# Kernel tuning notes

Hardware: AMD Instinct MI355X
Metric: run time of the kernel (lower is better)

## Reference

```python
import jax, jax.numpy as jnp
import numpy as np

INPUT_SIZE = 64
HIDDEN = 512
NUM_CLASSES = 10


def setup_inputs() -> dict:
    key = jax.random.key(0)
    ks = jax.random.split(key, 9)
    B, T = 1024, 256
    bound_lstm = 1.0 / np.sqrt(HIDDEN)
    bound_lin = 1.0 / np.sqrt(HIDDEN)
    x = jax.random.normal(ks[0], (B, T * INPUT_SIZE), dtype=jnp.float32)
    h0 = jax.random.normal(ks[1], (B, HIDDEN), dtype=jnp.float32)
    c0 = jax.random.normal(ks[2], (B, HIDDEN), dtype=jnp.float32)
    W_ih = jax.random.uniform(ks[3], (4 * HIDDEN, INPUT_SIZE), jnp.float32, -bound_lstm, bound_lstm)
    W_hh = jax.random.uniform(ks[4], (4 * HIDDEN, HIDDEN), jnp.float32, -bound_lstm, bound_lstm)
    b_ih = jax.random.uniform(ks[5], (4 * HIDDEN,), jnp.float32, -bound_lstm, bound_lstm)
    b_hh = jax.random.uniform(ks[6], (4 * HIDDEN,), jnp.float32, -bound_lstm, bound_lstm)
    W_lin = jax.random.uniform(ks[7], (NUM_CLASSES, HIDDEN), jnp.float32, -bound_lin, bound_lin)
    b_lin = jax.random.uniform(ks[8], (NUM_CLASSES,), jnp.float32, -bound_lin, bound_lin)
    return {"x": x, "h0": h0, "c0": c0, "W_ih": W_ih, "W_hh": W_hh,
            "b_ih": b_ih, "b_hh": b_hh, "W_lin": W_lin, "b_lin": b_lin}


def _lstm_forward(x, h0, c0, W_ih, W_hh, b_ih, b_hh, W_lin, b_lin):
    B = x.shape[0]
    T = x.shape[1] // INPUT_SIZE
    # [B, T*in] -> [T, B, in]; torch.split along dim 1 gives contiguous chunks
    xs = x.reshape(B, T, INPUT_SIZE).transpose(1, 0, 2)
    # precompute input projections for all steps: [T, B, 4H]
    gates_x = jnp.einsum('tbi,gi->tbg', xs, W_ih) + b_ih + b_hh

    def step(carry, gx):
        h, c = carry
        gates = gx + h @ W_hh.T  # [B, 4H], torch gate order i,f,g,o
        i, f, g, o = jnp.split(gates, 4, axis=-1)
        i = jax.nn.sigmoid(i)
        f = jax.nn.sigmoid(f)
        g = jnp.tanh(g)
        o = jax.nn.sigmoid(o)
        c_new = f * c + i * g
        h_new = o * jnp.tanh(c_new)
        return (h_new, c_new), None

    (hT, cT), _ = jax.lax.scan(step, (h0, c0), gates_x)
    preds = hT @ W_lin.T + b_lin  # [B, 10]
    return preds


def reference(x, h0, c0, W_ih, W_hh, b_ih, b_hh, W_lin, b_lin):
    return _lstm_forward(x, h0, c0, W_ih, W_hh, b_ih, b_hh, W_lin, b_lin)
```

## Files before the change

### kernel.cpp

```cpp
#include <hip/hip_runtime.h>
#include <hip/hip_bf16.h>


#define TST   256
#define BATCH 1024
#define HID   512
#define INSZ  64
#define NCLS  10
#define LDSTR 584

typedef _Float16 f16x8  __attribute__((ext_vector_type(8)));
typedef float    f32x16 __attribute__((ext_vector_type(16)));
typedef unsigned long long u64;

__device__ __forceinline__ float fast_rcp(float x) {
    return __builtin_amdgcn_rcpf(x);
}

__device__ __forceinline__ float tanh_f(float x) {
    return 2.0f * fast_rcp(1.0f + __expf(-2.0f * x)) - 1.0f;
}

__device__ __forceinline__ f16x8 cvt8(float4 a, float4 b) {
    f16x8 o;
    o[0] = (_Float16)a.x; o[1] = (_Float16)a.y; o[2] = (_Float16)a.z; o[3] = (_Float16)a.w;
    o[4] = (_Float16)b.x; o[5] = (_Float16)b.y; o[6] = (_Float16)b.z; o[7] = (_Float16)b.w;
    return o;
}

template <int CTRL>
__device__ __forceinline__ float dpp_f(float v) {
    return __builtin_bit_cast(float,
        __builtin_amdgcn_mov_dpp(__builtin_bit_cast(int, v), CTRL, 0xF, 0xF, true));
}
template <int CTRL>
__device__ __forceinline__ unsigned dpp_u(unsigned v) {
    return (unsigned)__builtin_amdgcn_mov_dpp((int)v, CTRL, 0xF, 0xF, true);
}

__global__ __launch_bounds__(256, 1) void lstm_persist(
    const float* __restrict__ x,   const float* __restrict__ h0,
    const float* __restrict__ c0,  const float* __restrict__ Wih,
    const float* __restrict__ Whh, const float* __restrict__ bih,
    const float* __restrict__ bhh, u64* __restrict__ hb)
{
    __shared__ __align__(16) _Float16 As[32][LDSTR];

    const int tid   = threadIdx.x;
    const int lane  = tid & 63;
    const int w     = tid >> 6;
    const int l31   = lane & 31;
    const int khalf = (lane >> 5) * 8;
    const int g  = (int)(blockIdx.x >> 3);
    const int jb = (int)(blockIdx.x & 7);
    const int m0 = g * 32;
    const int j0 = jb * 64;

    const int gate = l31 & 3;
    int jcol[2], nrow[2];
    #pragma unroll
    for (int nt = 0; nt < 2; ++nt) {
        int np = w * 64 + nt * 32 + l31;
        jcol[nt] = j0 + (np >> 2);
        nrow[nt] = gate * HID + jcol[nt];
    }

    f16x8 bfr[2][36];
    #pragma unroll
    for (int nt = 0; nt < 2; ++nt)
        #pragma unroll
        for (int kt = 0; kt < 36; ++kt) {
            const int k0 = kt * 16 + khalf;
            const float* p = (kt < 32) ? (Whh + (size_t)nrow[nt] * HID + k0)
                                       : (Wih + (size_t)nrow[nt] * INSZ + (k0 - HID));
            float4 f0 = ((const float4*)p)[0];
            float4 f1 = ((const float4*)p)[1];
            bfr[nt][kt] = cvt8(f0, f1);
        }
    float bsv[2];
    bsv[0] = bih[nrow[0]] + bhh[nrow[0]];
    bsv[1] = bih[nrow[1]] + bhh[nrow[1]];
    const float s   = (gate == 2) ? 2.0f : 1.0f;
    const int rowhi = (lane >> 5) * 4;

    float cr[2][16];
    #pragma unroll
    for (int nt = 0; nt < 2; ++nt)
        #pragma unroll
        for (int r = 0; r < 16; ++r) {
            int row = (r & 3) + 8 * (r >> 2) + rowhi;
            cr[nt][r] = c0[(size_t)(m0 + row) * HID + jcol[nt]];
        }

    const int rr = tid >> 3;
    const int q  = tid & 7;

    for (int t = 0; t < TST; ++t) {
        const u64* rb = hb + (size_t)((t + 2) % 3) * (BATCH * HID / 2);
        u64*       wb = hb + (size_t)(t % 3) * (BATCH * HID / 2);

        float4 x0, x1;
        {
            const float* xp = x + (size_t)(m0 + rr) * (TST * INSZ) + t * INSZ + q * 8;
            x0 = ((const float4*)xp)[0];
            x1 = ((const float4*)xp)[1];
        }
        if (t == 0) {
            #pragma unroll
            for (int u = 0; u < 16; ++u) {
                float4 f = *(const float4*)(h0 + (size_t)(m0 + rr) * HID + q * 4 + u * 32);
                _Float16 h4[4] = {(_Float16)f.x, (_Float16)f.y, (_Float16)f.z, (_Float16)f.w};
                u64 r8; __builtin_memcpy(&r8, h4, 8);
                *(u64*)&As[rr][q * 4 + u * 32] = r8;
            }
        } else {
            const unsigned tgt = (unsigned)t;
            const u64* rbq = rb + (size_t)(m0 + rr) * 256;
            u64 hv[32];
            int spins = 0;
            while (true) {
                unsigned bad = 0;
                #pragma unroll
                for (int u = 0; u < 32; ++u)
                    hv[u] = __hip_atomic_load(&rbq[q + u * 8],
                                              __ATOMIC_RELAXED, __HIP_MEMORY_SCOPE_AGENT);
                #pragma unroll
                for (int u = 0; u < 32; ++u)
                    bad |= ((unsigned)(hv[u] >> 32)) ^ tgt;
                if (__all((int)(bad == 0))) break;
                if (++spins > (1 << 14)) break;
                __builtin_amdgcn_s_sleep(8);
            }
            __atomic_signal_fence(__ATOMIC_SEQ_CST);
            #pragma unroll
            for (int u = 0; u < 32; ++u)
                *(unsigned*)&As[rr][(q + u * 8) * 2] = (unsigned)hv[u];
        }
        *(f16x8*)&As[rr][512 + q * 8] = cvt8(x0, x1);
        __syncthreads();

        f32x16 acc[2];
        #pragma unroll
        for (int i = 0; i < 16; ++i) { acc[0][i] = 0.0f; acc[1][i] = 0.0f; }
        #pragma unroll
        for (int kt = 0; kt < 36; ++kt) {
            f16x8 af = *(const f16x8*)&As[l31][kt * 16 + khalf];
            acc[0] = __builtin_amdgcn_mfma_f32_32x32x16_f16(af, bfr[0][kt], acc[0], 0, 0, 0);
            acc[1] = __builtin_amdgcn_mfma_f32_32x32x16_f16(af, bfr[1][kt], acc[1], 0, 0, 0);
        }

        const u64 tag64 = ((u64)(unsigned)(t + 1)) << 32;
        #pragma unroll
        for (int nt = 0; nt < 2; ++nt) {
            #pragma unroll
            for (int r = 0; r < 16; ++r) {
                float v = acc[nt][r] + bsv[nt];
                float e = __expf(-s * v);
                float act = s * fast_rcp(1.0f + e) - (s - 1.0f);
                float fu = dpp_f<0xB1>(act);
                float gu = dpp_f<0x4E>(act);
                float ou = dpp_f<0x1B>(act);
                float cn = fu * cr[nt][r] + act * gu;
                cr[nt][r] = cn;
                float hn = ou * tanh_f(cn);
                unsigned hu = (unsigned)__builtin_bit_cast(unsigned short, (_Float16)hn);
                unsigned pk = hu | (dpp_u<0x104>(hu) << 16);
                if ((l31 & 7) == 0) {
                    int row = (r & 3) + 8 * (r >> 2) + rowhi;
                    __hip_atomic_store(
                        wb + ((size_t)(m0 + row) * HID + jcol[nt]) / 2,
                        (u64)pk | tag64,
                        __ATOMIC_RELAXED, __HIP_MEMORY_SCOPE_AGENT);
                }
            }
        }
    }
}

__global__ __launch_bounds__(256) void final_kernel(
    const u64* __restrict__ h, const float* __restrict__ Wl,
    const float* __restrict__ bl, float* __restrict__ out)
{
    int i = blockIdx.x * 256 + threadIdx.x;
    if (i >= BATCH * NCLS) return;
    int b = i / NCLS, c = i - b * NCLS;
    const u64* hp = h + (size_t)b * (HID / 2);
    const float2* wp = (const float2*)(Wl + (size_t)c * HID);
    float sacc = bl[c];
    #pragma unroll 8
    for (int k2 = 0; k2 < HID / 2; ++k2) {
        unsigned lo = (unsigned)hp[k2];
        _Float16 h0v = __builtin_bit_cast(_Float16, (unsigned short)(lo & 0xFFFF));
        _Float16 h1v = __builtin_bit_cast(_Float16, (unsigned short)(lo >> 16));
        float2 wv = wp[k2];
        sacc += (float)h0v * wv.x + (float)h1v * wv.y;
    }
    out[i] = sacc;
}

extern "C" void kernel_launch(void* const* d_in, const int* in_sizes, int n_in,
                              void* d_out, int out_size, void* d_ws, size_t ws_size,
                              hipStream_t stream)
{
    const float* x    = (const float*)d_in[0];
    const float* h0   = (const float*)d_in[1];
    const float* c0   = (const float*)d_in[2];
    const float* Wih  = (const float*)d_in[3];
    const float* Whh  = (const float*)d_in[4];
    const float* bih  = (const float*)d_in[5];
    const float* bhh  = (const float*)d_in[6];
    const float* Wlin = (const float*)d_in[7];
    const float* blin = (const float*)d_in[8];
    float* out = (float*)d_out;

    u64* hb = (u64*)d_ws;

    hipMemsetAsync(d_ws, 0, 3 * (size_t)(BATCH * HID / 2) * 8, stream);

    lstm_persist<<<256, 256, 0, stream>>>(x, h0, c0, Wih, Whh, bih, bhh, hb);

    final_kernel<<<(BATCH * NCLS + 255) / 256, 256, 0, stream>>>(hb, Wlin, blin, out);
}
```

Baseline: 1.750 ms.

## Split batch rows into two ping-pong halves to overlap h polling with compute

Each block now owns two 16-row batch halves taken from far-apart batch groups instead of one 32-row group, and processes them alternately within each timestep. While one half computes, the next half's hidden-state loads are issued ahead of time, so the cross-block wait for the previous step's h overlaps with MFMA and activation work. In exchange, each half still issues full 32x32 MFMAs with only 16 useful rows, so matrix work per step doubles, and every step now has two block barriers.

```diff
diff --git a/kernel.cpp b/kernel.cpp
--- a/kernel.cpp
+++ b/kernel.cpp
@@ -16,18 +16,19 @@
 __device__ __forceinline__ float fast_rcp(float x) {
     return __builtin_amdgcn_rcpf(x);
 }
-
 __device__ __forceinline__ float tanh_f(float x) {
     return 2.0f * fast_rcp(1.0f + __expf(-2.0f * x)) - 1.0f;
 }
-
 __device__ __forceinline__ f16x8 cvt8(float4 a, float4 b) {
     f16x8 o;
     o[0] = (_Float16)a.x; o[1] = (_Float16)a.y; o[2] = (_Float16)a.z; o[3] = (_Float16)a.w;
     o[4] = (_Float16)b.x; o[5] = (_Float16)b.y; o[6] = (_Float16)b.z; o[7] = (_Float16)b.w;
     return o;
 }
-
+__device__ __forceinline__ u64 cvt4_u64(float4 a) {
+    _Float16 h[4] = {(_Float16)a.x, (_Float16)a.y, (_Float16)a.z, (_Float16)a.w};
+    u64 r; __builtin_memcpy(&r, h, 8); return r;
+}
 template <int CTRL>
 __device__ __forceinline__ float dpp_f(float v) {
     return __builtin_bit_cast(float,
@@ -44,17 +45,18 @@
     const float* __restrict__ Whh, const float* __restrict__ bih,
     const float* __restrict__ bhh, u64* __restrict__ hb)
 {
-    __shared__ __align__(16) _Float16 As[32][LDSTR];
+    __shared__ __align__(16) _Float16 As[2][32][LDSTR];
 
     const int tid   = threadIdx.x;
     const int lane  = tid & 63;
     const int w     = tid >> 6;
     const int l31   = lane & 31;
     const int khalf = (lane >> 5) * 8;
-    const int g  = (int)(blockIdx.x >> 3);
+    const int p  = (int)(blockIdx.x >> 3);
     const int jb = (int)(blockIdx.x & 7);
-    const int m0 = g * 32;
     const int j0 = jb * 64;
+    const int mbA = p * 16;
+    const int mbB = 512 + p * 16;
 
     const int gate = l31 & 3;
     int jcol[2], nrow[2];
@@ -71,10 +73,10 @@
         #pragma unroll
         for (int kt = 0; kt < 36; ++kt) {
             const int k0 = kt * 16 + khalf;
-            const float* p = (kt < 32) ? (Whh + (size_t)nrow[nt] * HID + k0)
-                                       : (Wih + (size_t)nrow[nt] * INSZ + (k0 - HID));
-            float4 f0 = ((const float4*)p)[0];
-            float4 f1 = ((const float4*)p)[1];
+            const float* ptr = (kt < 32) ? (Whh + (size_t)nrow[nt] * HID + k0)
+                                         : (Wih + (size_t)nrow[nt] * INSZ + (k0 - HID));
+            float4 f0 = ((const float4*)ptr)[0];
+            float4 f1 = ((const float4*)ptr)[1];
             bfr[nt][kt] = cvt8(f0, f1);
         }
     float bsv[2];
@@ -83,96 +85,188 @@
     const float s   = (gate == 2) ? 2.0f : 1.0f;
     const int rowhi = (lane >> 5) * 4;
 
-    float cr[2][16];
+    float cr[2][2][8];
     #pragma unroll
-    for (int nt = 0; nt < 2; ++nt)
+    for (int ch = 0; ch < 2; ++ch)
         #pragma unroll
-        for (int r = 0; r < 16; ++r) {
-            int row = (r & 3) + 8 * (r >> 2) + rowhi;
-            cr[nt][r] = c0[(size_t)(m0 + row) * HID + jcol[nt]];
-        }
-
-    const int rr = tid >> 3;
-    const int q  = tid & 7;
+        for (int nt = 0; nt < 2; ++nt)
+            #pragma unroll
+            for (int r = 0; r < 8; ++r) {
+                int row = (r & 3) + 8 * (r >> 2) + rowhi;
+                int mb  = ch ? mbB : mbA;
+                cr[ch][nt][r] = c0[(size_t)(mb + row) * HID + jcol[nt]];
+            }
+
+    const int rr = tid >> 4;
+    const int q  = tid & 15;
+
+    u64 hvA[16], hvB[16];
 
     for (int t = 0; t < TST; ++t) {
         const u64* rb = hb + (size_t)((t + 2) % 3) * (BATCH * HID / 2);
         u64*       wb = hb + (size_t)(t % 3) * (BATCH * HID / 2);
-
-        float4 x0, x1;
+        const u64 tag64 = ((u64)(unsigned)(t + 1)) << 32;
+        const unsigned tgt = (unsigned)t;
+
         {
-            const float* xp = x + (size_t)(m0 + rr) * (TST * INSZ) + t * INSZ + q * 8;
-            x0 = ((const float4*)xp)[0];
-            x1 = ((const float4*)xp)[1];
+            float4 xv = *(const float4*)(x + (size_t)(mbA + rr) * (TST * INSZ)
+                                           + t * INSZ + q * 4);
+            if (t == 0) {
+                #pragma unroll
+                for (int u = 0; u < 8; ++u) {
+                    float4 f = *(const float4*)(h0 + (size_t)(mbA + rr) * HID
+                                                  + q * 4 + u * 64);
+                    *(u64*)&As[0][rr][q * 4 + u * 64] = cvt4_u64(f);
+                }
+            } else {
+                const u64* rbq = rb + (size_t)(mbA + rr) * 256;
+                int spins = 0;
+                while (true) {
+                    unsigned bad = 0;
+                    #pragma unroll
+                    for (int u = 0; u < 16; ++u)
+                        bad |= ((unsigned)(hvA[u] >> 32)) ^ tgt;
+                    if (__all((int)(bad == 0))) break;
+                    if (++spins > (1 << 14)) break;
+                    __builtin_amdgcn_s_sleep(8);
+                    #pragma unroll
+                    for (int u = 0; u < 16; ++u)
+                        hvA[u] = __hip_atomic_load(&rbq[q + u * 16],
+                                                   __ATOMIC_RELAXED,
+                                                   __HIP_MEMORY_SCOPE_AGENT);
+                }
+                __atomic_signal_fence(__ATOMIC_SEQ_CST);
+                #pragma unroll
+                for (int u = 0; u < 16; ++u)
+                    *(unsigned*)&As[0][rr][(q + u * 16) * 2] = (unsigned)hvA[u];
+            }
+            *(u64*)&As[0][rr][512 + q * 4] = cvt4_u64(xv);
+            __syncthreads();
+
+            if (t >= 1) {
+                const u64* rbq = rb + (size_t)(mbB + rr) * 256;
+                #pragma unroll
+                for (int u = 0; u < 16; ++u)
+                    hvB[u] = __hip_atomic_load(&rbq[q + u * 16],
+                                               __ATOMIC_RELAXED,
+                                               __HIP_MEMORY_SCOPE_AGENT);
+                __atomic_signal_fence(__ATOMIC_SEQ_CST);
+            }
+
+            f32x16 acc[2];
+            #pragma unroll
+            for (int i = 0; i < 16; ++i) { acc[0][i] = 0.0f; acc[1][i] = 0.0f; }
+            #pragma unroll
+            for (int kt = 0; kt < 36; ++kt) {
+                f16x8 af = *(const f16x8*)&As[0][l31][kt * 16 + khalf];
+                acc[0] = __builtin_amdgcn_mfma_f32_32x32x16_f16(af, bfr[0][kt], acc[0], 0, 0, 0);
+                acc[1] = __builtin_amdgcn_mfma_f32_32x32x16_f16(af, bfr[1][kt], acc[1], 0, 0, 0);
+            }
+
+            #pragma unroll
+            for (int nt = 0; nt < 2; ++nt)
+                #pragma unroll
+                for (int r = 0; r < 8; ++r) {
+                    float v = acc[nt][r] + bsv[nt];
+                    float e = __expf(-s * v);
+                    float act = s * fast_rcp(1.0f + e) - (s - 1.0f);
+                    float fu = dpp_f<0xB1>(act);
+                    float gu = dpp_f<0x4E>(act);
+                    float ou = dpp_f<0x1B>(act);
+                    float cn = fu * cr[0][nt][r] + act * gu;
+                    cr[0][nt][r] = cn;
+                    float hn = ou * tanh_f(cn);
+                    unsigned hu = (unsigned)__builtin_bit_cast(unsigned short, (_Float16)hn);
+                    unsigned pk = hu | (dpp_u<0x104>(hu) << 16);
+                    if ((l31 & 7) == 0) {
+                        int row = (r & 3) + 8 * (r >> 2) + rowhi;
+                        __hip_atomic_store(
+                            wb + ((size_t)(mbA + row) * HID + jcol[nt]) / 2,
+                            (u64)pk | tag64,
+                            __ATOMIC_RELAXED, __HIP_MEMORY_SCOPE_AGENT);
+                    }
+                }
         }
-        if (t == 0) {
-            #pragma unroll
-            for (int u = 0; u < 16; ++u) {
-                float4 f = *(const float4*)(h0 + (size_t)(m0 + rr) * HID + q * 4 + u * 32);
-                _Float16 h4[4] = {(_Float16)f.x, (_Float16)f.y, (_Float16)f.z, (_Float16)f.w};
-                u64 r8; __builtin_memcpy(&r8, h4, 8);
-                *(u64*)&As[rr][q * 4 + u * 32] = r8;
-            }
-        } else {
-            const unsigned tgt = (unsigned)t;
-            const u64* rbq = rb + (size_t)(m0 + rr) * 256;
-            u64 hv[32];
-            int spins = 0;
-            while (true) {
-                unsigned bad = 0;
-                #pragma unroll
-                for (int u = 0; u < 32; ++u)
-                    hv[u] = __hip_atomic_load(&rbq[q + u * 8],
-                                              __ATOMIC_RELAXED, __HIP_MEMORY_SCOPE_AGENT);
-                #pragma unroll
-                for (int u = 0; u < 32; ++u)
-                    bad |= ((unsigned)(hv[u] >> 32)) ^ tgt;
-                if (__all((int)(bad == 0))) break;
-                if (++spins > (1 << 14)) break;
-                __builtin_amdgcn_s_sleep(8);
-            }
-            __atomic_signal_fence(__ATOMIC_SEQ_CST);
-            #pragma unroll
-            for (int u = 0; u < 32; ++u)
-                *(unsigned*)&As[rr][(q + u * 8) * 2] = (unsigned)hv[u];
-        }
-        *(f16x8*)&As[rr][512 + q * 8] = cvt8(x0, x1);
-        __syncthreads();
-
-        f32x16 acc[2];
-        #pragma unroll
-        for (int i = 0; i < 16; ++i) { acc[0][i] = 0.0f; acc[1][i] = 0.0f; }
-        #pragma unroll
-        for (int kt = 0; kt < 36; ++kt) {
-            f16x8 af = *(const f16x8*)&As[l31][kt * 16 + khalf];
-            acc[0] = __builtin_amdgcn_mfma_f32_32x32x16_f16(af, bfr[0][kt], acc[0], 0, 0, 0);
-            acc[1] = __builtin_amdgcn_mfma_f32_32x32x16_f16(af, bfr[1][kt], acc[1], 0, 0, 0);
-        }
-
-        const u64 tag64 = ((u64)(unsigned)(t + 1)) << 32;
-        #pragma unroll
-        for (int nt = 0; nt < 2; ++nt) {
-            #pragma unroll
-            for (int r = 0; r < 16; ++r) {
-                float v = acc[nt][r] + bsv[nt];
-                float e = __expf(-s * v);
-                float act = s * fast_rcp(1.0f + e) - (s - 1.0f);
-                float fu = dpp_f<0xB1>(act);
-                float gu = dpp_f<0x4E>(act);
-                float ou = dpp_f<0x1B>(act);
-                float cn = fu * cr[nt][r] + act * gu;
-                cr[nt][r] = cn;
-                float hn = ou * tanh_f(cn);
-                unsigned hu = (unsigned)__builtin_bit_cast(unsigned short, (_Float16)hn);
-                unsigned pk = hu | (dpp_u<0x104>(hu) << 16);
-                if ((l31 & 7) == 0) {
-                    int row = (r & 3) + 8 * (r >> 2) + rowhi;
-                    __hip_atomic_store(
-                        wb + ((size_t)(m0 + row) * HID + jcol[nt]) / 2,
-                        (u64)pk | tag64,
-                        __ATOMIC_RELAXED, __HIP_MEMORY_SCOPE_AGENT);
-                }
-            }
+
+        {
+            float4 xv = *(const float4*)(x + (size_t)(mbB + rr) * (TST * INSZ)
+                                           + t * INSZ + q * 4);
+            if (t == 0) {
+                #pragma unroll
+                for (int u = 0; u < 8; ++u) {
+                    float4 f = *(const float4*)(h0 + (size_t)(mbB + rr) * HID
+                                                  + q * 4 + u * 64);
+                    *(u64*)&As[1][rr][q * 4 + u * 64] = cvt4_u64(f);
+                }
+            } else {
+                const u64* rbq = rb + (size_t)(mbB + rr) * 256;
+                int spins = 0;
+                while (true) {
+                    unsigned bad = 0;
+                    #pragma unroll
+                    for (int u = 0; u < 16; ++u)
+                        bad |= ((unsigned)(hvB[u] >> 32)) ^ tgt;
+                    if (__all((int)(bad == 0))) break;
+                    if (++spins > (1 << 14)) break;
+                    __builtin_amdgcn_s_sleep(8);
+                    #pragma unroll
+                    for (int u = 0; u < 16; ++u)
+                        hvB[u] = __hip_atomic_load(&rbq[q + u * 16],
+                                                   __ATOMIC_RELAXED,
+                                                   __HIP_MEMORY_SCOPE_AGENT);
+                }
+                __atomic_signal_fence(__ATOMIC_SEQ_CST);
+                #pragma unroll
+                for (int u = 0; u < 16; ++u)
+                    *(unsigned*)&As[1][rr][(q + u * 16) * 2] = (unsigned)hvB[u];
+            }
+            *(u64*)&As[1][rr][512 + q * 4] = cvt4_u64(xv);
+            __syncthreads();
+
+            if (t < TST - 1) {
+                const u64* nbq = hb + (size_t)(t % 3) * (BATCH * HID / 2)
+                                    + (size_t)(mbA + rr) * 256;
+                #pragma unroll
+                for (int u = 0; u < 16; ++u)
+                    hvA[u] = __hip_atomic_load(&nbq[q + u * 16],
+                                               __ATOMIC_RELAXED,
+                                               __HIP_MEMORY_SCOPE_AGENT);
+                __atomic_signal_fence(__ATOMIC_SEQ_CST);
+            }
+
+            f32x16 acc[2];
+            #pragma unroll
+            for (int i = 0; i < 16; ++i) { acc[0][i] = 0.0f; acc[1][i] = 0.0f; }
+            #pragma unroll
+            for (int kt = 0; kt < 36; ++kt) {
+                f16x8 af = *(const f16x8*)&As[1][l31][kt * 16 + khalf];
+                acc[0] = __builtin_amdgcn_mfma_f32_32x32x16_f16(af, bfr[0][kt], acc[0], 0, 0, 0);
+                acc[1] = __builtin_amdgcn_mfma_f32_32x32x16_f16(af, bfr[1][kt], acc[1], 0, 0, 0);
+            }
+
+            #pragma unroll
+            for (int nt = 0; nt < 2; ++nt)
+                #pragma unroll
+                for (int r = 0; r < 8; ++r) {
+                    float v = acc[nt][r] + bsv[nt];
+                    float e = __expf(-s * v);
+                    float act = s * fast_rcp(1.0f + e) - (s - 1.0f);
+                    float fu = dpp_f<0xB1>(act);
+                    float gu = dpp_f<0x4E>(act);
+                    float ou = dpp_f<0x1B>(act);
+                    float cn = fu * cr[1][nt][r] + act * gu;
+                    cr[1][nt][r] = cn;
+                    float hn = ou * tanh_f(cn);
+                    unsigned hu = (unsigned)__builtin_bit_cast(unsigned short, (_Float16)hn);
+                    unsigned pk = hu | (dpp_u<0x104>(hu) << 16);
+                    if ((l31 & 7) == 0) {
+                        int row = (r & 3) + 8 * (r >> 2) + rowhi;
+                        __hip_atomic_store(
+                            wb + ((size_t)(mbB + row) * HID + jcol[nt]) / 2,
+                            (u64)pk | tag64,
+                            __ATOMIC_RELAXED, __HIP_MEMORY_SCOPE_AGENT);
+                    }
+                }
         }
     }
 }
```

New measurement: 4.116 ms. 135% more time.

## Pipeline hidden-state wait with MFMA compute in k-chunks and double-buffer LDS

Applied to the files above, without the earlier changes.

Splits the per-timestep spin-wait on the recurrent hidden state into eight chunks, each followed by a workgroup barrier and the MFMAs for that chunk of K. Compute can then begin as soon as the first part of h is published, rather than after all of it. The LDS A tile is double-buffered by timestep parity so the next step's writes do not clash with reads of the previous one. In exchange there are more barriers per step, and the loop over kt has a non-constant trip count, which risks dynamic indexing into the bfr register array and spills to scratch.

```diff
diff --git a/kernel.cpp b/kernel.cpp
--- a/kernel.cpp
+++ b/kernel.cpp
@@ -16,18 +16,19 @@
 __device__ __forceinline__ float fast_rcp(float x) {
     return __builtin_amdgcn_rcpf(x);
 }
-
 __device__ __forceinline__ float tanh_f(float x) {
     return 2.0f * fast_rcp(1.0f + __expf(-2.0f * x)) - 1.0f;
 }
-
 __device__ __forceinline__ f16x8 cvt8(float4 a, float4 b) {
     f16x8 o;
     o[0] = (_Float16)a.x; o[1] = (_Float16)a.y; o[2] = (_Float16)a.z; o[3] = (_Float16)a.w;
     o[4] = (_Float16)b.x; o[5] = (_Float16)b.y; o[6] = (_Float16)b.z; o[7] = (_Float16)b.w;
     return o;
 }
-
+__device__ __forceinline__ u64 cvt4_u64(float4 a) {
+    _Float16 h[4] = {(_Float16)a.x, (_Float16)a.y, (_Float16)a.z, (_Float16)a.w};
+    u64 r; __builtin_memcpy(&r, h, 8); return r;
+}
 template <int CTRL>
 __device__ __forceinline__ float dpp_f(float v) {
     return __builtin_bit_cast(float,
@@ -36,6 +37,12 @@
 template <int CTRL>
 __device__ __forceinline__ unsigned dpp_u(unsigned v) {
     return (unsigned)__builtin_amdgcn_mov_dpp((int)v, CTRL, 0xF, 0xF, true);
+}
+
+__device__ __forceinline__ void phase_barrier() {
+    asm volatile("s_waitcnt lgkmcnt(0)" ::: "memory");
+    __builtin_amdgcn_s_barrier();
+    asm volatile("" ::: "memory");
 }
 
 __global__ __launch_bounds__(256, 1) void lstm_persist(
@@ -44,7 +51,7 @@
     const float* __restrict__ Whh, const float* __restrict__ bih,
     const float* __restrict__ bhh, u64* __restrict__ hb)
 {
-    __shared__ __align__(16) _Float16 As[32][LDSTR];
+    __shared__ __align__(16) _Float16 As[2][32][LDSTR];
 
     const int tid   = threadIdx.x;
     const int lane  = tid & 63;
@@ -98,58 +105,71 @@
     for (int t = 0; t < TST; ++t) {
         const u64* rb = hb + (size_t)((t + 2) % 3) * (BATCH * HID / 2);
         u64*       wb = hb + (size_t)(t % 3) * (BATCH * HID / 2);
-
-        float4 x0, x1;
+        const unsigned tgt = (unsigned)t;
+        const u64 tag64 = ((u64)(unsigned)(t + 1)) << 32;
+        const int buf = t & 1;
+        const u64* rbq = rb + (size_t)(m0 + rr) * 256;
+
+        u64 hv[32];
+        if (t > 0) {
+            #pragma unroll
+            for (int u = 0; u < 32; ++u)
+                hv[u] = __hip_atomic_load(&rbq[q + u * 8],
+                                          __ATOMIC_RELAXED, __HIP_MEMORY_SCOPE_AGENT);
+        }
+
         {
             const float* xp = x + (size_t)(m0 + rr) * (TST * INSZ) + t * INSZ + q * 8;
-            x0 = ((const float4*)xp)[0];
-            x1 = ((const float4*)xp)[1];
+            float4 x0 = ((const float4*)xp)[0];
+            float4 x1 = ((const float4*)xp)[1];
+            *(f16x8*)&As[buf][rr][512 + q * 8] = cvt8(x0, x1);
         }
         if (t == 0) {
             #pragma unroll
             for (int u = 0; u < 16; ++u) {
                 float4 f = *(const float4*)(h0 + (size_t)(m0 + rr) * HID + q * 4 + u * 32);
-                _Float16 h4[4] = {(_Float16)f.x, (_Float16)f.y, (_Float16)f.z, (_Float16)f.w};
-                u64 r8; __builtin_memcpy(&r8, h4, 8);
-                *(u64*)&As[rr][q * 4 + u * 32] = r8;
-            }
-        } else {
-            const unsigned tgt = (unsigned)t;
-            const u64* rbq = rb + (size_t)(m0 + rr) * 256;
-            u64 hv[32];
-            int spins = 0;
-            while (true) {
-                unsigned bad = 0;
+                *(u64*)&As[buf][rr][q * 4 + u * 32] = cvt4_u64(f);
+            }
+        }
+
+        f32x16 acc[2];
+        #pragma unroll
+        for (int i = 0; i < 16; ++i) { acc[0][i] = 0.0f; acc[1][i] = 0.0f; }
+
+        #pragma unroll
+        for (int j = 0; j < 8; ++j) {
+            if (t > 0) {
+                int spins = 0;
+                while (true) {
+                    unsigned bad = 0;
+                    #pragma unroll
+                    for (int u = 0; u < 4; ++u)
+                        bad |= ((unsigned)(hv[j * 4 + u] >> 32)) ^ tgt;
+                    if (__all((int)(bad == 0))) break;
+                    if (++spins > (1 << 14)) break;
+                    __builtin_amdgcn_s_sleep(8);
+                    #pragma unroll
+                    for (int u = 0; u < 4; ++u)
+                        hv[j * 4 + u] = __hip_atomic_load(&rbq[q + (j * 4 + u) * 8],
+                                                          __ATOMIC_RELAXED,
+                                                          __HIP_MEMORY_SCOPE_AGENT);
+                }
+                __atomic_signal_fence(__ATOMIC_SEQ_CST);
                 #pragma unroll
-                for (int u = 0; u < 32; ++u)
-                    hv[u] = __hip_atomic_load(&rbq[q + u * 8],
-                                              __ATOMIC_RELAXED, __HIP_MEMORY_SCOPE_AGENT);
-                #pragma unroll
-                for (int u = 0; u < 32; ++u)
-                    bad |= ((unsigned)(hv[u] >> 32)) ^ tgt;
-                if (__all((int)(bad == 0))) break;
-                if (++spins > (1 << 14)) break;
-                __builtin_amdgcn_s_sleep(8);
-            }
-            __atomic_signal_fence(__ATOMIC_SEQ_CST);
-            #pragma unroll
-            for (int u = 0; u < 32; ++u)
-                *(unsigned*)&As[rr][(q + u * 8) * 2] = (unsigned)hv[u];
-        }
-        *(f16x8*)&As[rr][512 + q * 8] = cvt8(x0, x1);
-        __syncthreads();
-
-        f32x16 acc[2];
-        #pragma unroll
-        for (int i = 0; i < 16; ++i) { acc[0][i] = 0.0f; acc[1][i] = 0.0f; }
-        #pragma unroll
-        for (int kt = 0; kt < 36; ++kt) {
-            f16x8 af = *(const f16x8*)&As[l31][kt * 16 + khalf];
-            acc[0] = __builtin_amdgcn_mfma_f32_32x32x16_f16(af, bfr[0][kt], acc[0], 0, 0, 0);
-            acc[1] = __builtin_amdgcn_mfma_f32_32x32x16_f16(af, bfr[1][kt], acc[1], 0, 0, 0);
-        }
-
-        const u64 tag64 = ((u64)(unsigned)(t + 1)) << 32;
+                for (int u = 0; u < 4; ++u)
+                    *(unsigned*)&As[buf][rr][(q + (j * 4 + u) * 8) * 2] =
+                        (unsigned)hv[j * 4 + u];
+            }
+            phase_barrier();
+
+            const int ktEnd = (j == 7) ? 36 : (j * 4 + 4);
+            for (int kt = j * 4; kt < ktEnd; ++kt) {
+                f16x8 af = *(const f16x8*)&As[buf][l31][kt * 16 + khalf];
+                acc[0] = __builtin_amdgcn_mfma_f32_32x32x16_f16(af, bfr[0][kt], acc[0], 0, 0, 0);
+                acc[1] = __builtin_amdgcn_mfma_f32_32x32x16_f16(af, bfr[1][kt], acc[1], 0, 0, 0);
+            }
+        }
+
         #pragma unroll
         for (int nt = 0; nt < 2; ++nt) {
             #pragma unroll
```

Measured after the change: 2.294 ms. +31.1%, slower.
